# Performance work log

Hardware: AMD Instinct MI355X
Metric: run time of the kernel (lower is better)

## Reference

```python
import jax, jax.numpy as jnp
import numpy as np

B, T, CIN, CH, M, NCLS = 2048, 8, 2048, 1024, 32, 21
EPS = 1e-8  # torch.cosine_similarity eps


def setup_inputs() -> dict:
    key = jax.random.key(0)
    ks = jax.random.split(key, 16)
    g = lambda k, shp, sc=0.02: jax.random.normal(k, shp, dtype=jnp.float32) * sc
    return {
        "x": g(ks[0], (B, T, CIN), 1.0),
        "static_feat": g(ks[1], (NCLS, CIN, M), 1.0),  # 21 kmeans exemplar banks
        "Wk": g(ks[2], (CH, CIN)), "bk": g(ks[3], (CH,)),
        "Wv": g(ks[4], (CH, CIN)), "bv": g(ks[5], (CH,)),
        "WEk": g(ks[6], (CH, CIN)), "bEk": g(ks[7], (CH,)),
        "WEv": g(ks[8], (CH, CIN)), "bEv": g(ks[9], (CH,)),
        "Ww": g(ks[10], (1, CH)), "bw": g(ks[11], (1,)),
        "Wout": g(ks[12], (NCLS, 2 * CH)), "bout": g(ks[13], (NCLS,)),
    }


def reference(x, static_feat, Wk, bk, Wv, bv, WEk, bEk, WEv, bEv, Ww, bw, Wout, bout):
    # last frame only: [B, CIN]
    xl = x[:, -1, :]
    # 1x1 convs on length-1 sequence == dense projections
    k = xl @ Wk.T + bk          # [B, CH]
    v = xl @ Wv.T + bv          # [B, CH]
    # project all 21 static memories at once: [NCLS, CH, M]
    Ek = jnp.einsum('oc,ncm->nom', WEk, static_feat) + bEk[None, :, None]
    Ev = jnp.einsum('oc,ncm->nom', WEv, static_feat) + bEv[None, :, None]
    # cosine similarity along channel dim (torch clamps each norm at eps)
    kn = k / jnp.maximum(jnp.linalg.norm(k, axis=1, keepdims=True), EPS)
    Ekn = Ek / jnp.maximum(jnp.linalg.norm(Ek, axis=1, keepdims=True), EPS)
    cos = jnp.einsum('bo,nom->bnm', kn, Ekn)      # [B, NCLS, M]
    w = jax.nn.softmax(cos, axis=-1)               # softmax over exemplars
    s = jnp.einsum('nom,bnm->bno', Ev, w)          # weighted sums [B, NCLS, CH]
    # per-class scalar weights via conv2_1_W, softmax over the 21 classes
    fw = jax.nn.softmax(s @ Ww[0] + bw[0], axis=-1)  # [B, NCLS]
    fE = jnp.einsum('bno,bn->bo', s, fw)             # [B, CH]
    h = jax.nn.relu(jnp.concatenate([v, fE], axis=-1))  # [B, 2*CH]
    out = h @ Wout.T + bout                              # [B, NCLS]
    return out[:, :, None]  # [B, NCLS, 1] to match Conv1d output
```

## Files before the change

### kernel.cpp

```cpp
#include <hip/hip_runtime.h>
#include <math.h>

#define B_    2048
#define T_    8
#define CIN_  2048
#define CH_   1024
#define M_    32
#define NCLS_ 21
#define NM_   (NCLS_*M_)
#define NMP_  768
#define EPS_  1e-8f

typedef __bf16 bf16_t;
typedef bf16_t bf16x4 __attribute__((ext_vector_type(4)));
typedef bf16_t bf16x8 __attribute__((ext_vector_type(8)));
typedef float  floatx4 __attribute__((ext_vector_type(4)));

#define GLOBAL_AS __attribute__((address_space(1)))
#define LDS_AS    __attribute__((address_space(3)))

__global__ __launch_bounds__(256) void gemm128(
    const bf16_t* __restrict__ A0, const bf16_t* __restrict__ A1, int msplit,
    const bf16_t* __restrict__ B0, const bf16_t* __restrict__ B1,
    const float* __restrict__ bias0, const float* __restrict__ bias1,
    int ld, float* __restrict__ C, int ldc, size_t strideC, int mzero, int Ksplit)
{
  __shared__ bf16_t As[128 * 64];
  __shared__ bf16_t Bs[128 * 64];
  const int tid = threadIdx.x;
  const int n0 = blockIdx.x * 128, m0 = blockIdx.y * 128;
  const int z = blockIdx.z;

  const bf16_t* A; const bf16_t* B; const float* bias; int mrow;
  if (m0 < msplit) { A = A0; B = B0; bias = bias0; mrow = m0; }
  else             { A = A1; B = B1; bias = bias1; mrow = m0 - msplit; }
  const int koff = z * Ksplit;

  const int w = tid >> 6, lane = tid & 63;
  const int srow = lane >> 3;
  const int sblk = (lane & 7) ^ srow;
  const bf16_t* ga = A + (size_t)(mrow + w * 32 + srow) * ld + koff + sblk * 8;
  const bf16_t* gb = B + (size_t)(n0   + w * 32 + srow) * ld + koff + sblk * 8;

  const int wm = (w >> 1) * 64, wn = (w & 1) * 64;
  const int l15 = lane & 15, quad = lane >> 4;
  const int sx = l15 & 7;

  floatx4 acc[4][4] = {};

  for (int k0 = 0; k0 < Ksplit; k0 += 64) {
    __syncthreads();
    #pragma unroll
    for (int q = 0; q < 4; ++q) {
      __builtin_amdgcn_global_load_lds(
          (const GLOBAL_AS void*)(ga + (size_t)q * 8 * ld),
          (LDS_AS void*)(&As[(w * 4 + q) * 512]), 16, 0, 0);
      __builtin_amdgcn_global_load_lds(
          (const GLOBAL_AS void*)(gb + (size_t)q * 8 * ld),
          (LDS_AS void*)(&Bs[(w * 4 + q) * 512]), 16, 0, 0);
    }
    ga += 64; gb += 64;
    __syncthreads();
    #pragma unroll
    for (int ks = 0; ks < 2; ++ks) {
      bf16x8 af[4], bfr[4];
      #pragma unroll
      for (int i = 0; i < 4; ++i)
        af[i] = *(const bf16x8*)(&As[(wm + i * 16 + l15) * 64 + ((ks * 4 + quad) ^ sx) * 8]);
      #pragma unroll
      for (int j = 0; j < 4; ++j)
        bfr[j] = *(const bf16x8*)(&Bs[(wn + j * 16 + l15) * 64 + ((ks * 4 + quad) ^ sx) * 8]);
      #pragma unroll
      for (int i = 0; i < 4; ++i)
        #pragma unroll
        for (int j = 0; j < 4; ++j)
          acc[i][j] = __builtin_amdgcn_mfma_f32_16x16x32_bf16(af[i], bfr[j], acc[i][j], 0, 0, 0);
    }
  }

  float* Cz = C + (size_t)z * strideC;
  #pragma unroll
  for (int i = 0; i < 4; ++i) {
    const int rbase = m0 + wm + i * 16 + quad * 4;
    #pragma unroll
    for (int j = 0; j < 4; ++j) {
      const int c = n0 + wn + j * 16 + l15;
      const float badd = (bias && z == 0) ? bias[c] : 0.f;
      #pragma unroll
      for (int r = 0; r < 4; ++r) {
        const int rr = rbase + r;
        float v = acc[i][j][r] + badd;
        if (rr >= mzero) v = 0.f;
        Cz[(size_t)rr * ldc + c] = v;
      }
    }
  }
}

template<int MODE>
__global__ __launch_bounds__(256) void gemm_n64(
    const bf16_t* __restrict__ A, const bf16_t* __restrict__ B, int ld,
    float* __restrict__ C, bf16_t* __restrict__ Cb, int ldc, size_t strideC,
    int Ksplit)
{
  __shared__ bf16_t As[128 * 64];
  __shared__ bf16_t Bs[64 * 64];
  const int tid = threadIdx.x;
  const int n0 = blockIdx.x * 64, m0 = blockIdx.y * 128;
  const int z = blockIdx.z;
  const int koff = z * Ksplit;

  const int w = tid >> 6, lane = tid & 63;
  const int srow = lane >> 3;
  const int sblk = (lane & 7) ^ srow;
  const bf16_t* ga = A + (size_t)(m0 + w * 32 + srow) * ld + koff + sblk * 8;
  const bf16_t* gb = B + (size_t)(n0 + w * 16 + srow) * ld + koff + sblk * 8;

  const int l15 = lane & 15, quad = lane >> 4;
  const int sx = l15 & 7;

  floatx4 acc[2][4] = {};

  for (int k0 = 0; k0 < Ksplit; k0 += 64) {
    __syncthreads();
    #pragma unroll
    for (int q = 0; q < 4; ++q)
      __builtin_amdgcn_global_load_lds(
          (const GLOBAL_AS void*)(ga + (size_t)q * 8 * ld),
          (LDS_AS void*)(&As[(w * 4 + q) * 512]), 16, 0, 0);
    #pragma unroll
    for (int q = 0; q < 2; ++q)
      __builtin_amdgcn_global_load_lds(
          (const GLOBAL_AS void*)(gb + (size_t)q * 8 * ld),
          (LDS_AS void*)(&Bs[(w * 2 + q) * 512]), 16, 0, 0);
    ga += 64; gb += 64;
    __syncthreads();
    #pragma unroll
    for (int ks = 0; ks < 2; ++ks) {
      bf16x8 af[2], bfr[4];
      #pragma unroll
      for (int i = 0; i < 2; ++i)
        af[i] = *(const bf16x8*)(&As[(w * 32 + i * 16 + l15) * 64 + ((ks * 4 + quad) ^ sx) * 8]);
      #pragma unroll
      for (int j = 0; j < 4; ++j)
        bfr[j] = *(const bf16x8*)(&Bs[(j * 16 + l15) * 64 + ((ks * 4 + quad) ^ sx) * 8]);
      #pragma unroll
      for (int i = 0; i < 2; ++i)
        #pragma unroll
        for (int j = 0; j < 4; ++j)
          acc[i][j] = __builtin_amdgcn_mfma_f32_16x16x32_bf16(af[i], bfr[j], acc[i][j], 0, 0, 0);
    }
  }

  #pragma unroll
  for (int i = 0; i < 2; ++i) {
    const int rbase = m0 + w * 32 + i * 16 + quad * 4;
    #pragma unroll
    for (int j = 0; j < 4; ++j) {
      const int c = n0 + j * 16 + l15;
      #pragma unroll
      for (int r = 0; r < 4; ++r) {
        const int rr = rbase + r;
        if (MODE == 0)
          (C + (size_t)z * strideC)[(size_t)rr * ldc + c] = acc[i][j][r];
        else
          Cb[(size_t)rr * ldc + c] = (bf16_t)fmaxf(acc[i][j][r], 0.f);
      }
    }
  }
}

__global__ __launch_bounds__(256) void kPrep(
    const float* __restrict__ x, const float* __restrict__ Wk,
    const float* __restrict__ Wv, const float* __restrict__ WEk,
    const float* __restrict__ WEv, const float* __restrict__ bk,
    const float* __restrict__ bv, const float* __restrict__ bEk,
    const float* __restrict__ bEv, const float* __restrict__ Wout,
    bf16_t* __restrict__ xb, bf16_t* __restrict__ Wkvb, bf16_t* __restrict__ WEb,
    bf16_t* __restrict__ Woutb, float* __restrict__ bkv, float* __restrict__ bE)
{
  const int blk = blockIdx.x;
  if (blk == 3072) {
    for (int i = threadIdx.x; i < CH_; i += 256) {
      bkv[i] = bk[i]; bkv[CH_ + i] = bv[i];
      bE[i]  = bEk[i]; bE[CH_ + i] = bEv[i];
    }
    return;
  }
  if (blk > 3072) {
    const size_t e0 = ((size_t)(blk - 3073) * 256 + threadIdx.x) * 16;
    if (e0 < (size_t)NCLS_ * 2 * CH_) {
      #pragma unroll
      for (int q = 0; q < 4; ++q) {
        const float4 v = *(const float4*)(Wout + e0 + q * 4);
        bf16x4 o = { (bf16_t)v.x, (bf16_t)v.y, (bf16_t)v.z, (bf16_t)v.w };
        *(bf16x4*)(Woutb + e0 + q * 4) = o;
      }
    }
    return;
  }
  const int sec = blk >> 10;
  const int t = ((blk & 1023) << 8) + threadIdx.x;
  const size_t e0 = (size_t)t * 16;
  const int row = (int)(e0 >> 11);
  const int col = (int)(e0 & 2047);
  const float* src;
  bf16_t* dst;
  if (sec == 0) {
    src = x + (size_t)row * (T_ * CIN_) + (size_t)(T_ - 1) * CIN_ + col;
    dst = xb + e0;
  } else if (sec == 1) {
    src = (row < CH_ ? Wk + (size_t)row * CIN_ : Wv + (size_t)(row - CH_) * CIN_) + col;
    dst = Wkvb + e0;
  } else {
    src = (row < CH_ ? WEk + (size_t)row * CIN_ : WEv + (size_t)(row - CH_) * CIN_) + col;
    dst = WEb + e0;
  }
  #pragma unroll
  for (int q = 0; q < 4; ++q) {
    const float4 v = *(const float4*)(src + q * 4);
    bf16x4 o = { (bf16_t)v.x, (bf16_t)v.y, (bf16_t)v.z, (bf16_t)v.w };
    *(bf16x4*)(dst + q * 4) = o;
  }
}

__global__ __launch_bounds__(256) void kTrSf(
    const float* __restrict__ sf, bf16_t* __restrict__ sfTb)
{
  __shared__ float t[32][33];
  const int nn = blockIdx.x;
  const int c0 = blockIdx.y * 32;
  const int tid = threadIdx.x;
  const int cc = tid & 31, r8 = tid >> 5;
  #pragma unroll
  for (int q = 0; q < 4; ++q) {
    const int cl = r8 + q * 8;
    float v = 0.f;
    if (nn < NCLS_) v = sf[((size_t)nn * CIN_ + c0 + cl) * M_ + cc];
    t[cl][cc] = v;
  }
  __syncthreads();
  #pragma unroll
  for (int q = 0; q < 4; ++q) {
    const int ml = r8 + q * 8;
    sfTb[(size_t)(nn * 32 + ml) * CIN_ + c0 + cc] = (bf16_t)t[cc][ml];
  }
}

__global__ __launch_bounds__(64) void kNormKE(
    const float* __restrict__ KVE0, const float* __restrict__ KVE1,
    const float* __restrict__ Ww,
    bf16_t* __restrict__ knb, bf16_t* __restrict__ Eknb, float* __restrict__ EvW)
{
  const int r = blockIdx.x;
  const int lane = threadIdx.x;
  const float* r0 = KVE0 + (size_t)r * 2048;
  const float* r1 = KVE1 + (size_t)r * 2048;
  float vals[16];
  float ss = 0.f;
  #pragma unroll
  for (int i = 0; i < 16; ++i) {
    const int o = lane + i * 64;
    const float v = r0[o] + r1[o];
    vals[i] = v;
    ss += v * v;
  }
  for (int off = 32; off; off >>= 1) ss += __shfl_xor(ss, off);
  const float inv = 1.f / fmaxf(sqrtf(ss), EPS_);
  bf16_t* dst = (r < B_) ? knb + (size_t)r * CH_ : Eknb + (size_t)(r - B_) * CH_;
  #pragma unroll
  for (int i = 0; i < 16; ++i) dst[lane + i * 64] = (bf16_t)(vals[i] * inv);
  if (r >= B_) {
    float dd = 0.f;
    for (int o = lane; o < CH_; o += 64)
      dd += (r0[CH_ + o] + r1[CH_ + o]) * Ww[o];
    for (int off = 32; off; off >>= 1) dd += __shfl_xor(dd, off);
    if (lane == 0) EvW[r - B_] = dd;
  }
}

__global__ __launch_bounds__(256) void kTrEv(
    const float* __restrict__ KVE0, const float* __restrict__ KVE1,
    bf16_t* __restrict__ Ev2b)
{
  __shared__ float t[32][33];
  const int nm0 = blockIdx.x * 32;
  const int o0 = blockIdx.y * 32;
  const int tid = threadIdx.x;
  const int cc = tid & 31, r8 = tid >> 5;
  #pragma unroll
  for (int q = 0; q < 4; ++q) {
    const int r = r8 + q * 8;
    const size_t idx = (size_t)(B_ + nm0 + r) * 2048 + CH_ + o0 + cc;
    t[r][cc] = KVE0[idx] + KVE1[idx];
  }
  __syncthreads();
  #pragma unroll
  for (int q = 0; q < 4; ++q) {
    const int r = r8 + q * 8;
    Ev2b[(size_t)(o0 + r) * NMP_ + nm0 + cc] = (bf16_t)t[cc][r];
  }
}

__global__ __launch_bounds__(256) void kSoftmax(
    const float* __restrict__ cosb0, const float* __restrict__ cosb1,
    const float* __restrict__ EvW, const float* __restrict__ bw,
    bf16_t* __restrict__ wwb)
{
  const int b = blockIdx.x;
  const int tid = threadIdx.x;
  __shared__ float sc[NM_];
  __shared__ float sl[NCLS_];
  for (int i = tid; i < NM_; i += 256)
    sc[i] = cosb0[(size_t)b * NMP_ + i] + cosb1[(size_t)b * NMP_ + i];
  __syncthreads();
  if (tid < NCLS_) {
    const int base = tid * M_;
    float mx = -1e30f;
    for (int m = 0; m < M_; ++m) mx = fmaxf(mx, sc[base + m]);
    float s = 0.f;
    for (int m = 0; m < M_; ++m) {
      const float e = __expf(sc[base + m] - mx);
      sc[base + m] = e;
      s += e;
    }
    const float inv = 1.f / s;
    float lg = 0.f;
    for (int m = 0; m < M_; ++m) {
      const float w = sc[base + m] * inv;
      sc[base + m] = w;
      lg += w * EvW[base + m];
    }
    sl[tid] = lg + bw[0];
  }
  __syncthreads();
  if (tid == 0) {
    float mx = -1e30f;
    for (int n = 0; n < NCLS_; ++n) mx = fmaxf(mx, sl[n]);
    float s = 0.f;
    for (int n = 0; n < NCLS_; ++n) { const float e = __expf(sl[n] - mx); sl[n] = e; s += e; }
    const float inv = 1.f / s;
    for (int n = 0; n < NCLS_; ++n) sl[n] *= inv;
  }
  __syncthreads();
  for (int i = tid; i < NMP_; i += 256) {
    const float v = (i < NM_) ? sc[i] * sl[i >> 5] : 0.f;
    wwb[(size_t)b * NMP_ + i] = (bf16_t)v;
  }
}

__global__ __launch_bounds__(256) void kOut(
    const float* __restrict__ KVE0, const float* __restrict__ KVE1,
    const bf16_t* __restrict__ fEb, const bf16_t* __restrict__ Woutb,
    const float* __restrict__ bout, float* __restrict__ out)
{
  const int b = blockIdx.x;
  const int tid = threadIdx.x;
  __shared__ float h[2 * CH_];
  for (int j = tid; j < CH_; j += 256) {
    const size_t idx = (size_t)b * 2048 + CH_ + j;
    h[j] = fmaxf(KVE0[idx] + KVE1[idx], 0.f);
  }
  for (int j = tid; j < CH_; j += 256)
    h[CH_ + j] = (float)fEb[(size_t)b * CH_ + j];
  __syncthreads();
  const int wave = tid >> 6, lane = tid & 63;
  for (int n = wave; n < NCLS_; n += 4) {
    const bf16_t* wr = Woutb + (size_t)n * (2 * CH_);
    float s = 0.f;
    for (int j = lane; j < 2 * CH_; j += 64) s += h[j] * (float)wr[j];
    for (int off = 32; off; off >>= 1) s += __shfl_xor(s, off);
    if (lane == 0) out[(size_t)b * NCLS_ + n] = s + bout[n];
  }
}

extern "C" void kernel_launch(void* const* d_in, const int* in_sizes, int n_in,
                              void* d_out, int out_size, void* d_ws, size_t ws_size,
                              hipStream_t stream)
{
  const float* x    = (const float*)d_in[0];
  const float* sf   = (const float*)d_in[1];
  const float* Wk   = (const float*)d_in[2];
  const float* bk   = (const float*)d_in[3];
  const float* Wv   = (const float*)d_in[4];
  const float* bv   = (const float*)d_in[5];
  const float* WEk  = (const float*)d_in[6];
  const float* bEk  = (const float*)d_in[7];
  const float* WEv  = (const float*)d_in[8];
  const float* bEv  = (const float*)d_in[9];
  const float* Ww   = (const float*)d_in[10];
  const float* bw   = (const float*)d_in[11];
  const float* Wout = (const float*)d_in[12];
  const float* bout = (const float*)d_in[13];
  float* out = (float*)d_out;

  char* ws = (char*)d_ws;
  size_t off = 0;
  auto alloc = [&](size_t bytes) { char* p = ws + off; off += (bytes + 255) & ~(size_t)255; return p; };
  float*  KVE0  = (float*)alloc((size_t)2816 * 2048 * 4);
  float*  KVE1  = (float*)alloc((size_t)2816 * 2048 * 4);
  bf16_t* xb    = (bf16_t*)alloc((size_t)2048 * 2048 * 2);
  bf16_t* Wkvb  = (bf16_t*)alloc((size_t)2048 * 2048 * 2);
  bf16_t* WEb   = (bf16_t*)alloc((size_t)2048 * 2048 * 2);
  bf16_t* sfTb  = (bf16_t*)alloc((size_t)NMP_ * 2048 * 2);
  bf16_t* knb   = (bf16_t*)alloc((size_t)B_ * CH_ * 2);
  bf16_t* Eknb  = (bf16_t*)alloc((size_t)NMP_ * CH_ * 2);
  bf16_t* Ev2b  = (bf16_t*)alloc((size_t)CH_ * NMP_ * 2);
  float*  cosb0 = (float*)alloc((size_t)B_ * NMP_ * 4);
  float*  cosb1 = (float*)alloc((size_t)B_ * NMP_ * 4);
  bf16_t* wwb   = (bf16_t*)alloc((size_t)B_ * NMP_ * 2);
  bf16_t* fEb   = (bf16_t*)alloc((size_t)B_ * CH_ * 2);
  bf16_t* Woutb = (bf16_t*)alloc((size_t)NCLS_ * 2 * CH_ * 2);
  float*  bkv   = (float*)alloc(2 * CH_ * 4);
  float*  bE    = (float*)alloc(2 * CH_ * 4);
  float*  EvW   = (float*)alloc(NMP_ * 4);

  kPrep<<<3084, 256, 0, stream>>>(x, Wk, Wv, WEk, WEv, bk, bv, bEk, bEv, Wout,
                                  xb, Wkvb, WEb, Woutb, bkv, bE);
  kTrSf<<<dim3(24, CIN_ / 32), 256, 0, stream>>>(sf, sfTb);
  gemm128<<<dim3(16, 22, 2), 256, 0, stream>>>(
      xb, sfTb, B_, Wkvb, WEb, bkv, bE, CIN_,
      KVE0, 2048, (size_t)(KVE1 - KVE0), B_ + NM_, CIN_ / 2);
  kNormKE<<<B_ + NMP_, 64, 0, stream>>>(KVE0, KVE1, Ww, knb, Eknb, EvW);
  kTrEv<<<dim3(NMP_ / 32, CH_ / 32), 256, 0, stream>>>(KVE0, KVE1, Ev2b);
  gemm_n64<0><<<dim3(NMP_ / 64, 16, 2), 256, 0, stream>>>(
      knb, Eknb, CH_, cosb0, nullptr, NMP_, (size_t)(cosb1 - cosb0), CH_ / 2);
  kSoftmax<<<B_, 256, 0, stream>>>(cosb0, cosb1, EvW, bw, wwb);
  gemm_n64<1><<<dim3(CH_ / 64, 16, 1), 256, 0, stream>>>(
      wwb, Ev2b, NMP_, nullptr, fEb, CH_, 0, NMP_);
  kOut<<<B_, 256, 0, stream>>>(KVE0, KVE1, fEb, Woutb, bout, out);
}
```

Before: 358.7 us.

## Raise split-K to four for projection GEMM and merge small kernels

The main projection GEMM now uses four K-splits instead of two, with partial results held in one strided buffer, which gives more workgroups on the 704-tile grid. The sf transpose is folded into the prep kernel, and the norm and Ev transpose kernels are merged into one launch, cutting the launch count by two. The cost is twice the fp32 partial-sum traffic: every consumer of KVE now reads four partials instead of two.

```diff
diff --git a/kernel.cpp b/kernel.cpp
--- a/kernel.cpp
+++ b/kernel.cpp
@@ -10,6 +10,8 @@
 #define NM_   (NCLS_*M_)
 #define NMP_  768
 #define EPS_  1e-8f
+#define ZKV_  4
+#define ZC_   2
 
 typedef __bf16 bf16_t;
 typedef bf16_t bf16x4 __attribute__((ext_vector_type(4)));
@@ -170,25 +172,50 @@
   }
 }
 
-__global__ __launch_bounds__(256) void kPrep(
+__global__ __launch_bounds__(256) void kPrepAll(
     const float* __restrict__ x, const float* __restrict__ Wk,
     const float* __restrict__ Wv, const float* __restrict__ WEk,
     const float* __restrict__ WEv, const float* __restrict__ bk,
     const float* __restrict__ bv, const float* __restrict__ bEk,
     const float* __restrict__ bEv, const float* __restrict__ Wout,
+    const float* __restrict__ sf,
     bf16_t* __restrict__ xb, bf16_t* __restrict__ Wkvb, bf16_t* __restrict__ WEb,
-    bf16_t* __restrict__ Woutb, float* __restrict__ bkv, float* __restrict__ bE)
-{
+    bf16_t* __restrict__ Woutb, bf16_t* __restrict__ sfTb,
+    float* __restrict__ bkv, float* __restrict__ bE)
+{
+  __shared__ float t[32][33];
   const int blk = blockIdx.x;
+  const int tid = threadIdx.x;
+
+  if (blk >= 3084) {
+    const int tt = blk - 3084;
+    const int nn = tt % 24;
+    const int c0 = (tt / 24) * 32;
+    const int cc = tid & 31, r8 = tid >> 5;
+    #pragma unroll
+    for (int q = 0; q < 4; ++q) {
+      const int cl = r8 + q * 8;
+      float v = 0.f;
+      if (nn < NCLS_) v = sf[((size_t)nn * CIN_ + c0 + cl) * M_ + cc];
+      t[cl][cc] = v;
+    }
+    __syncthreads();
+    #pragma unroll
+    for (int q = 0; q < 4; ++q) {
+      const int ml = r8 + q * 8;
+      sfTb[(size_t)(nn * 32 + ml) * CIN_ + c0 + cc] = (bf16_t)t[cc][ml];
+    }
+    return;
+  }
   if (blk == 3072) {
-    for (int i = threadIdx.x; i < CH_; i += 256) {
+    for (int i = tid; i < CH_; i += 256) {
       bkv[i] = bk[i]; bkv[CH_ + i] = bv[i];
       bE[i]  = bEk[i]; bE[CH_ + i] = bEv[i];
     }
     return;
   }
   if (blk > 3072) {
-    const size_t e0 = ((size_t)(blk - 3073) * 256 + threadIdx.x) * 16;
+    const size_t e0 = ((size_t)(blk - 3073) * 256 + tid) * 16;
     if (e0 < (size_t)NCLS_ * 2 * CH_) {
       #pragma unroll
       for (int q = 0; q < 4; ++q) {
@@ -200,8 +227,8 @@
     return;
   }
   const int sec = blk >> 10;
-  const int t = ((blk & 1023) << 8) + threadIdx.x;
-  const size_t e0 = (size_t)t * 16;
+  const int tt = ((blk & 1023) << 8) + tid;
+  const size_t e0 = (size_t)tt * 16;
   const int row = (int)(e0 >> 11);
   const int col = (int)(e0 & 2047);
   const float* src;
@@ -224,75 +251,60 @@
   }
 }
 
-__global__ __launch_bounds__(256) void kTrSf(
-    const float* __restrict__ sf, bf16_t* __restrict__ sfTb)
+__global__ __launch_bounds__(256) void kNormTr(
+    const float* __restrict__ KVE, size_t PS, const float* __restrict__ Ww,
+    bf16_t* __restrict__ knb, bf16_t* __restrict__ Eknb, float* __restrict__ EvW,
+    bf16_t* __restrict__ Ev2b)
 {
   __shared__ float t[32][33];
-  const int nn = blockIdx.x;
-  const int c0 = blockIdx.y * 32;
-  const int tid = threadIdx.x;
-  const int cc = tid & 31, r8 = tid >> 5;
-  #pragma unroll
-  for (int q = 0; q < 4; ++q) {
-    const int cl = r8 + q * 8;
-    float v = 0.f;
-    if (nn < NCLS_) v = sf[((size_t)nn * CIN_ + c0 + cl) * M_ + cc];
-    t[cl][cc] = v;
-  }
-  __syncthreads();
-  #pragma unroll
-  for (int q = 0; q < 4; ++q) {
-    const int ml = r8 + q * 8;
-    sfTb[(size_t)(nn * 32 + ml) * CIN_ + c0 + cc] = (bf16_t)t[cc][ml];
-  }
-}
-
-__global__ __launch_bounds__(64) void kNormKE(
-    const float* __restrict__ KVE0, const float* __restrict__ KVE1,
-    const float* __restrict__ Ww,
-    bf16_t* __restrict__ knb, bf16_t* __restrict__ Eknb, float* __restrict__ EvW)
-{
-  const int r = blockIdx.x;
-  const int lane = threadIdx.x;
-  const float* r0 = KVE0 + (size_t)r * 2048;
-  const float* r1 = KVE1 + (size_t)r * 2048;
-  float vals[16];
-  float ss = 0.f;
-  #pragma unroll
-  for (int i = 0; i < 16; ++i) {
-    const int o = lane + i * 64;
-    const float v = r0[o] + r1[o];
-    vals[i] = v;
-    ss += v * v;
-  }
-  for (int off = 32; off; off >>= 1) ss += __shfl_xor(ss, off);
-  const float inv = 1.f / fmaxf(sqrtf(ss), EPS_);
-  bf16_t* dst = (r < B_) ? knb + (size_t)r * CH_ : Eknb + (size_t)(r - B_) * CH_;
-  #pragma unroll
-  for (int i = 0; i < 16; ++i) dst[lane + i * 64] = (bf16_t)(vals[i] * inv);
-  if (r >= B_) {
-    float dd = 0.f;
-    for (int o = lane; o < CH_; o += 64)
-      dd += (r0[CH_ + o] + r1[CH_ + o]) * Ww[o];
-    for (int off = 32; off; off >>= 1) dd += __shfl_xor(dd, off);
-    if (lane == 0) EvW[r - B_] = dd;
-  }
-}
-
-__global__ __launch_bounds__(256) void kTrEv(
-    const float* __restrict__ KVE0, const float* __restrict__ KVE1,
-    bf16_t* __restrict__ Ev2b)
-{
-  __shared__ float t[32][33];
-  const int nm0 = blockIdx.x * 32;
-  const int o0 = blockIdx.y * 32;
-  const int tid = threadIdx.x;
+  const int blk = blockIdx.x;
+  const int tid = threadIdx.x;
+
+  if (blk < 704) {
+    const int r = blk * 4 + (tid >> 6);
+    const int lane = tid & 63;
+    const float* row = KVE + (size_t)r * 2048;
+    float vals[16];
+    float ss = 0.f;
+    #pragma unroll
+    for (int i = 0; i < 16; ++i) {
+      const int o = lane + i * 64;
+      float v = row[o];
+      #pragma unroll
+      for (int z = 1; z < ZKV_; ++z) v += row[(size_t)z * PS + o];
+      vals[i] = v;
+      ss += v * v;
+    }
+    for (int off = 32; off; off >>= 1) ss += __shfl_xor(ss, off);
+    const float inv = 1.f / fmaxf(sqrtf(ss), EPS_);
+    bf16_t* dst = (r < B_) ? knb + (size_t)r * CH_ : Eknb + (size_t)(r - B_) * CH_;
+    #pragma unroll
+    for (int i = 0; i < 16; ++i) dst[lane + i * 64] = (bf16_t)(vals[i] * inv);
+    if (r >= B_) {
+      float dd = 0.f;
+      for (int o = lane; o < CH_; o += 64) {
+        float v = row[CH_ + o];
+        #pragma unroll
+        for (int z = 1; z < ZKV_; ++z) v += row[(size_t)z * PS + CH_ + o];
+        dd += v * Ww[o];
+      }
+      for (int off = 32; off; off >>= 1) dd += __shfl_xor(dd, off);
+      if (lane == 0) EvW[r - B_] = dd;
+    }
+    return;
+  }
+  const int tt = blk - 704;
+  const int nm0 = (tt % 24) * 32;
+  const int o0 = (tt / 24) * 32;
   const int cc = tid & 31, r8 = tid >> 5;
   #pragma unroll
   for (int q = 0; q < 4; ++q) {
     const int r = r8 + q * 8;
     const size_t idx = (size_t)(B_ + nm0 + r) * 2048 + CH_ + o0 + cc;
-    t[r][cc] = KVE0[idx] + KVE1[idx];
+    float v = KVE[idx];
+    #pragma unroll
+    for (int z = 1; z < ZKV_; ++z) v += KVE[(size_t)z * PS + idx];
+    t[r][cc] = v;
   }
   __syncthreads();
   #pragma unroll
@@ -303,7 +315,7 @@
 }
 
 __global__ __launch_bounds__(256) void kSoftmax(
-    const float* __restrict__ cosb0, const float* __restrict__ cosb1,
+    const float* __restrict__ cosb, size_t PSc,
     const float* __restrict__ EvW, const float* __restrict__ bw,
     bf16_t* __restrict__ wwb)
 {
@@ -311,8 +323,12 @@
   const int tid = threadIdx.x;
   __shared__ float sc[NM_];
   __shared__ float sl[NCLS_];
-  for (int i = tid; i < NM_; i += 256)
-    sc[i] = cosb0[(size_t)b * NMP_ + i] + cosb1[(size_t)b * NMP_ + i];
+  for (int i = tid; i < NM_; i += 256) {
+    float v = cosb[(size_t)b * NMP_ + i];
+    #pragma unroll
+    for (int z = 1; z < ZC_; ++z) v += cosb[(size_t)z * PSc + (size_t)b * NMP_ + i];
+    sc[i] = v;
+  }
   __syncthreads();
   if (tid < NCLS_) {
     const int base = tid * M_;
@@ -350,7 +366,7 @@
 }
 
 __global__ __launch_bounds__(256) void kOut(
-    const float* __restrict__ KVE0, const float* __restrict__ KVE1,
+    const float* __restrict__ KVE, size_t PS,
     const bf16_t* __restrict__ fEb, const bf16_t* __restrict__ Woutb,
     const float* __restrict__ bout, float* __restrict__ out)
 {
@@ -359,7 +375,10 @@
   __shared__ float h[2 * CH_];
   for (int j = tid; j < CH_; j += 256) {
     const size_t idx = (size_t)b * 2048 + CH_ + j;
-    h[j] = fmaxf(KVE0[idx] + KVE1[idx], 0.f);
+    float v = KVE[idx];
+    #pragma unroll
+    for (int z = 1; z < ZKV_; ++z) v += KVE[(size_t)z * PS + idx];
+    h[j] = fmaxf(v, 0.f);
   }
   for (int j = tid; j < CH_; j += 256)
     h[CH_ + j] = (float)fEb[(size_t)b * CH_ + j];
@@ -397,8 +416,9 @@
   char* ws = (char*)d_ws;
   size_t off = 0;
   auto alloc = [&](size_t bytes) { char* p = ws + off; off += (bytes + 255) & ~(size_t)255; return p; };
-  float*  KVE0  = (float*)alloc((size_t)2816 * 2048 * 4);
-  float*  KVE1  = (float*)alloc((size_t)2816 * 2048 * 4);
+  const size_t PS  = (size_t)2816 * 2048;
+  const size_t PSc = (size_t)B_ * NMP_;
+  float*  KVE   = (float*)alloc(PS * ZKV_ * 4);
   bf16_t* xb    = (bf16_t*)alloc((size_t)2048 * 2048 * 2);
   bf16_t* Wkvb  = (bf16_t*)alloc((size_t)2048 * 2048 * 2);
   bf16_t* WEb   = (bf16_t*)alloc((size_t)2048 * 2048 * 2);
@@ -406,8 +426,7 @@
   bf16_t* knb   = (bf16_t*)alloc((size_t)B_ * CH_ * 2);
   bf16_t* Eknb  = (bf16_t*)alloc((size_t)NMP_ * CH_ * 2);
   bf16_t* Ev2b  = (bf16_t*)alloc((size_t)CH_ * NMP_ * 2);
-  float*  cosb0 = (float*)alloc((size_t)B_ * NMP_ * 4);
-  float*  cosb1 = (float*)alloc((size_t)B_ * NMP_ * 4);
+  float*  cosb  = (float*)alloc(PSc * ZC_ * 4);
   bf16_t* wwb   = (bf16_t*)alloc((size_t)B_ * NMP_ * 2);
   bf16_t* fEb   = (bf16_t*)alloc((size_t)B_ * CH_ * 2);
   bf16_t* Woutb = (bf16_t*)alloc((size_t)NCLS_ * 2 * CH_ * 2);
@@ -415,18 +434,17 @@
   float*  bE    = (float*)alloc(2 * CH_ * 4);
   float*  EvW   = (float*)alloc(NMP_ * 4);
 
-  kPrep<<<3084, 256, 0, stream>>>(x, Wk, Wv, WEk, WEv, bk, bv, bEk, bEv, Wout,
-                                  xb, Wkvb, WEb, Woutb, bkv, bE);
-  kTrSf<<<dim3(24, CIN_ / 32), 256, 0, stream>>>(sf, sfTb);
-  gemm128<<<dim3(16, 22, 2), 256, 0, stream>>>(
+  kPrepAll<<<4620, 256, 0, stream>>>(x, Wk, Wv, WEk, WEv, bk, bv, bEk, bEv,
+                                     Wout, sf, xb, Wkvb, WEb, Woutb, sfTb,
+                                     bkv, bE);
+  gemm128<<<dim3(16, 22, ZKV_), 256, 0, stream>>>(
       xb, sfTb, B_, Wkvb, WEb, bkv, bE, CIN_,
-      KVE0, 2048, (size_t)(KVE1 - KVE0), B_ + NM_, CIN_ / 2);
-  kNormKE<<<B_ + NMP_, 64, 0, stream>>>(KVE0, KVE1, Ww, knb, Eknb, EvW);
-  kTrEv<<<dim3(NMP_ / 32, CH_ / 32), 256, 0, stream>>>(KVE0, KVE1, Ev2b);
-  gemm_n64<0><<<dim3(NMP_ / 64, 16, 2), 256, 0, stream>>>(
-      knb, Eknb, CH_, cosb0, nullptr, NMP_, (size_t)(cosb1 - cosb0), CH_ / 2);
-  kSoftmax<<<B_, 256, 0, stream>>>(cosb0, cosb1, EvW, bw, wwb);
+      KVE, 2048, PS, B_ + NM_, CIN_ / ZKV_);
+  kNormTr<<<1472, 256, 0, stream>>>(KVE, PS, Ww, knb, Eknb, EvW, Ev2b);
+  gemm_n64<0><<<dim3(NMP_ / 64, 16, ZC_), 256, 0, stream>>>(
+      knb, Eknb, CH_, cosb, nullptr, NMP_, PSc, CH_ / ZC_);
+  kSoftmax<<<B_, 256, 0, stream>>>(cosb, PSc, EvW, bw, wwb);
   gemm_n64<1><<<dim3(CH_ / 64, 16, 1), 256, 0, stream>>>(
       wwb, Ev2b, NMP_, nullptr, fEb, CH_, 0, NMP_);
-  kOut<<<B_, 256, 0, stream>>>(KVE0, KVE1, fEb, Woutb, bout, out);
-}
+  kOut<<<B_, 256, 0, stream>>>(KVE, PS, fEb, Woutb, bout, out);
+}
```

Result: slower. 369.9 us (+3.1%).
